# Performance work log

Measured on AMD Instinct MI355X. Metric: run time of the kernel, lower is better.

## Reference

```python
import jax, jax.numpy as jnp
import numpy as np

DELTA = 1e-3  # inverse-distance kernel smoothing from NEC paper
NUM_NEIGHBOURS = 50


def setup_inputs() -> dict:
    key = jax.random.key(0)
    k1, k2, k3 = jax.random.split(key, 3)
    B, C, D = 1024, 500000, 64
    return {
        "keys": jax.random.normal(k1, (B, D), dtype=jnp.float32),
        "table_keys": jax.random.normal(k2, (C, D), dtype=jnp.float32),
        "table_values": jax.random.normal(k3, (C,), dtype=jnp.float32),
    }


def reference(keys, table_keys, table_values):
    # Brute-force kNN search: squared L2 distances [B, C]
    d2 = (
        jnp.sum(keys * keys, axis=1, keepdims=True)
        - 2.0 * (keys @ table_keys.T)
        + jnp.sum(table_keys * table_keys, axis=1)[None, :]
    )
    _, idx = jax.lax.top_k(-d2, NUM_NEIGHBOURS)  # [B, K] smallest distances

    neighbours = table_keys[idx]  # [B, K, D] gather
    # recompute exact squared distances against gathered neighbours
    sq = jnp.sum((keys[:, None, :] - neighbours) ** 2, axis=2)  # [B, K]
    w = 1.0 / (sq + DELTA)
    w = w / jnp.sum(w, axis=1, keepdims=True)
    v = table_values[idx]  # [B, K]
    return jnp.sum(w * v, axis=1)  # [B]
```

## Files before the change

### kernel.cpp

```cpp
#include <hip/hip_runtime.h>
#include <math.h>


#define DELTA_SMOOTH 1e-3f
#define K_NEIGH 50
#define MAXCAP 8192
#define SAMPLE 2048
#define SAMPLE_TARGET 6
#define NBINS 256
#define MARGIN 0.75f
#define MARGIN_Q 26
#define RPB 1024
#define QTILE 512
#define SDEPTH 8
#define LW 768
#define NQ 1024

typedef __attribute__((ext_vector_type(8))) short short8;
typedef __attribute__((ext_vector_type(4))) float f32x4;

__device__ __forceinline__ unsigned f2bf(float f) {
  unsigned u = __float_as_uint(f);
  return ((u + 0x7fffu + ((u >> 16) & 1u)) >> 16) & 0xffffu;
}

__global__ __launch_bounds__(256) void qthresh_kernel(
    const float* __restrict__ keys, const float* __restrict__ tk,
    float* __restrict__ thr, float* __restrict__ qnorm, int C) {
  int q = blockIdx.x;
  __shared__ __align__(16) float kq[64];
  __shared__ unsigned hist[NBINS];
  __shared__ float qn_sh;
  __shared__ unsigned wsum[4];
  __shared__ int bstar_sh;
  int tid = threadIdx.x;
  int lane = tid & 63;
  int wid = tid >> 6;
  if (tid < 64) kq[tid] = keys[(size_t)q * 64 + tid];
  hist[tid] = 0u;
  if (tid == 0) bstar_sh = NBINS - 1;
  __syncthreads();
  if (tid < 64) {
    float v = kq[tid];
    float s = v * v;
    #pragma unroll
    for (int off = 32; off > 0; off >>= 1) s += __shfl_down(s, off);
    if (tid == 0) qn_sh = s;
  }
  __syncthreads();
  float qn = qn_sh;
  int kc = lane & 3;
  const float4* kq4 = (const float4*)kq;
  float4 kf[4];
  #pragma unroll
  for (int j = 0; j < 4; ++j) kf[j] = kq4[kc * 4 + j];
  int S = SAMPLE < C ? SAMPLE : C;
  for (int r = wid * (S >> 2) + (lane >> 2); r < (wid + 1) * (S >> 2); r += 16) {
    const float4* trow = (const float4*)(tk + (size_t)r * 64 + kc * 16);
    float a0 = 0.f, a1 = 0.f, sq = 0.f;
    #pragma unroll
    for (int j = 0; j < 4; ++j) {
      float4 tvv = trow[j];
      float4 kv = kf[j];
      a0 += kv.x * tvv.x + kv.y * tvv.y;
      a1 += kv.z * tvv.z + kv.w * tvv.w;
      sq += tvv.x * tvv.x + tvv.y * tvv.y + tvv.z * tvv.z + tvv.w * tvv.w;
    }
    float s = a0 + a1;
    s += __shfl_xor(s, 1); s += __shfl_xor(s, 2);
    sq += __shfl_xor(sq, 1); sq += __shfl_xor(sq, 2);
    if (kc == 0) {
      float d2 = qn + sq - 2.f * s;
      int b = (int)d2;
      b = b < 0 ? 0 : (b > NBINS - 1 ? NBINS - 1 : b);
      atomicAdd(&hist[b], 1u);
    }
  }
  __syncthreads();
  unsigned h = hist[tid];
  unsigned p = h;
  #pragma unroll
  for (int off = 1; off < 64; off <<= 1) {
    unsigned v = __shfl_up(p, off);
    if (lane >= off) p += v;
  }
  if (lane == 63) wsum[wid] = p;
  __syncthreads();
  unsigned add = 0;
  for (int w2 = 0; w2 < wid; ++w2) add += wsum[w2];
  p += add;
  if (p >= (unsigned)SAMPLE_TARGET && p - h < (unsigned)SAMPLE_TARGET) bstar_sh = tid;
  __syncthreads();
  if (tid == 0) {
    thr[q] = (float)(bstar_sh + 1) + MARGIN - qn;
    qnorm[q] = qn;
  }
}

__global__ __launch_bounds__(512, 4) void filter_mfma_kernel(
    const float* __restrict__ keys, const float* __restrict__ tk,
    const float* __restrict__ thr, const float* __restrict__ qnorm,
    int* __restrict__ cnt, unsigned* __restrict__ candi, int C, int cap) {
  __shared__ float tnstage[64];
  __shared__ float thr_lds[QTILE];
  __shared__ float qn_lds[QTILE];
  __shared__ unsigned scnt[QTILE];
  __shared__ unsigned sbuf[QTILE * SDEPTH];
  __shared__ __align__(16) unsigned char bstage[64 * 128];

  int tid = threadIdx.x;
  int qt = blockIdx.x & 1;
  int chunk = blockIdx.x >> 1;
  int qbase = qt * QTILE;
  int rstart = chunk * RPB;

  thr_lds[tid] = thr[qbase + tid];
  qn_lds[tid] = qnorm[qbase + tid];
  scnt[tid] = 0u;

  int lane = tid & 63;
  int wq = tid >> 6;
  int l15 = lane & 15;
  int quad = lane >> 4;

  short8 afrag[4][2];
  #pragma unroll
  for (int mt = 0; mt < 4; ++mt) {
    const float* kp = keys + (size_t)(qbase + wq * 64 + mt * 16 + l15) * 64 + quad * 8;
    #pragma unroll
    for (int s = 0; s < 2; ++s) {
      float4 x = *(const float4*)(kp + s * 32);
      float4 y = *(const float4*)(kp + s * 32 + 4);
      short8 a;
      a[0] = (short)f2bf(x.x); a[1] = (short)f2bf(x.y);
      a[2] = (short)f2bf(x.z); a[3] = (short)f2bf(x.w);
      a[4] = (short)f2bf(y.x); a[5] = (short)f2bf(y.y);
      a[6] = (short)f2bf(y.z); a[7] = (short)f2bf(y.w);
      afrag[mt][s] = a;
    }
  }
  __syncthreads();

  float hq[4];
  #pragma unroll
  for (int mt = 0; mt < 4; ++mt) {
    float h0 = thr_lds[wq * 64 + mt * 16 + quad * 4 + 0];
    float h1 = thr_lds[wq * 64 + mt * 16 + quad * 4 + 1];
    float h2 = thr_lds[wq * 64 + mt * 16 + quad * 4 + 2];
    float h3 = thr_lds[wq * 64 + mt * 16 + quad * 4 + 3];
    hq[mt] = fmaxf(fmaxf(h0, h1), fmaxf(h2, h3));
  }

  int srow = tid >> 3;
  int scol = tid & 7;
  unsigned sbyte = (unsigned)(srow * 128 + ((scol ^ (srow & 7)) << 4));

  const int ITERS = RPB / 64;
  int r0 = rstart + srow; if (r0 > C - 1) r0 = C - 1;
  float4 pa = *(const float4*)(tk + (size_t)r0 * 64 + scol * 8);
  float4 pb = *(const float4*)(tk + (size_t)r0 * 64 + scol * 8 + 4);

  f32x4 zero4 = {0.f, 0.f, 0.f, 0.f};

  for (int it = 0; it < ITERS; ++it) {
    float part = pa.x * pa.x + pa.y * pa.y + pa.z * pa.z + pa.w * pa.w
               + pb.x * pb.x + pb.y * pb.y + pb.z * pb.z + pb.w * pb.w;
    part += __shfl_xor(part, 1);
    part += __shfl_xor(part, 2);
    part += __shfl_xor(part, 4);
    if ((tid & 7) == 0) tnstage[srow] = part;
    uint4 u;
    u.x = f2bf(pa.x) | (f2bf(pa.y) << 16);
    u.y = f2bf(pa.z) | (f2bf(pa.w) << 16);
    u.z = f2bf(pb.x) | (f2bf(pb.y) << 16);
    u.w = f2bf(pb.z) | (f2bf(pb.w) << 16);
    *(uint4*)(bstage + sbyte) = u;
    __syncthreads();
    if (it + 1 < ITERS) {
      int rn = rstart + (it + 1) * 64 + srow; if (rn > C - 1) rn = C - 1;
      pa = *(const float4*)(tk + (size_t)rn * 64 + scol * 8);
      pb = *(const float4*)(tk + (size_t)rn * 64 + scol * 8 + 4);
    }
    #pragma unroll
    for (int half = 0; half < 2; ++half) {
      short8 b[2][2];
      #pragma unroll
      for (int tt = 0; tt < 2; ++tt) {
        int nloc = half * 32 + tt * 16 + l15;
        #pragma unroll
        for (int s = 0; s < 2; ++s) {
          int c = s * 4 + quad;
          unsigned addr = (unsigned)(nloc * 128 + ((c ^ (nloc & 7)) << 4));
          b[tt][s] = *(const short8*)(bstage + addr);
        }
      }
      f32x4 acc[4][2];
      #pragma unroll
      for (int mt = 0; mt < 4; ++mt) {
        #pragma unroll
        for (int tt = 0; tt < 2; ++tt) {
          f32x4 a0 = __builtin_amdgcn_mfma_f32_16x16x32_bf16(afrag[mt][0], b[tt][0], zero4, 0, 0, 0);
          acc[mt][tt] = __builtin_amdgcn_mfma_f32_16x16x32_bf16(afrag[mt][1], b[tt][1], a0, 0, 0, 0);
        }
      }
      #pragma unroll
      for (int tt = 0; tt < 2; ++tt) {
        float tn = tnstage[half * 32 + tt * 16 + l15];
        int n = rstart + it * 64 + half * 32 + tt * 16 + l15;
        #pragma unroll
        for (int mt = 0; mt < 4; ++mt) {
          float d0 = fmaf(-2.f, acc[mt][tt][0], tn);
          float d1 = fmaf(-2.f, acc[mt][tt][1], tn);
          float d2 = fmaf(-2.f, acc[mt][tt][2], tn);
          float d3 = fmaf(-2.f, acc[mt][tt][3], tn);
          float mn4 = fminf(fminf(d0, d1), fminf(d2, d3));
          if (mn4 < hq[mt]) {
            float dd[4] = {d0, d1, d2, d3};
            #pragma unroll
            for (int r = 0; r < 4; ++r) {
              int ql = wq * 64 + mt * 16 + quad * 4 + r;
              if (dd[r] < thr_lds[ql] && n < C) {
                float d2f = dd[r] + qn_lds[ql];
                int d2q = (int)(d2f * 16.f);
                d2q = d2q < 0 ? 0 : (d2q > 8191 ? 8191 : d2q);
                unsigned v = ((unsigned)d2q << 19) | (unsigned)n;
                unsigned p = atomicAdd(&scnt[ql], 1u);
                if (p < SDEPTH) {
                  sbuf[ql * SDEPTH + p] = v;
                } else {
                  int g = atomicAdd(&cnt[qbase + ql], 1);
                  if (g < cap) candi[(size_t)(qbase + ql) * cap + g] = v;
                }
              }
            }
          }
        }
      }
    }
    __syncthreads();
  }
  int m = (int)scnt[tid];
  if (m > SDEPTH) m = SDEPTH;
  if (m > 0) {
    int base = atomicAdd(&cnt[qbase + tid], m);
    for (int j = 0; j < m; ++j) {
      int g = base + j;
      if (g < cap) candi[(size_t)(qbase + tid) * cap + g] = sbuf[tid * SDEPTH + j];
    }
  }
}

__global__ __launch_bounds__(256) void select_kernel(
    const float* __restrict__ keys, const float* __restrict__ tk,
    const float* __restrict__ tv, const int* __restrict__ cnt,
    const unsigned* __restrict__ candi, float* __restrict__ out, int cap) {
  int q = blockIdx.x;
  __shared__ unsigned hist[NBINS];
  __shared__ unsigned wsum[4];
  __shared__ unsigned minq_sh;
  __shared__ int b50_sh;
  __shared__ int lidx[LW];
  __shared__ unsigned ed2[LW];
  __shared__ int m_sh;
  __shared__ float redw[4], redwv[4];
  int tid = threadIdx.x;
  int lane = tid & 63;
  int wid = tid >> 6;
  int n = cnt[q];
  if (n > cap) n = cap;
  hist[tid] = 0u;
  if (tid == 0) { minq_sh = 0xffffffffu; b50_sh = NBINS - 1; m_sh = 0; }
  __syncthreads();
  const unsigned* cv = candi + (size_t)q * cap;
  unsigned mn = 0xffffffffu;
  for (int i = tid; i < n; i += 256) { unsigned d = cv[i] >> 19; if (d < mn) mn = d; }
  #pragma unroll
  for (int off = 1; off < 64; off <<= 1) { unsigned o = __shfl_xor(mn, off); if (o < mn) mn = o; }
  if (lane == 0) atomicMin(&minq_sh, mn);
  __syncthreads();
  unsigned base = minq_sh;
  for (int i = tid; i < n; i += 256) {
    unsigned d = (cv[i] >> 19) - base;
    unsigned b = d >> 1; if (b > NBINS - 1) b = NBINS - 1;
    atomicAdd(&hist[b], 1u);
  }
  __syncthreads();
  unsigned h = hist[tid];
  unsigned p = h;
  #pragma unroll
  for (int off = 1; off < 64; off <<= 1) {
    unsigned v = __shfl_up(p, off);
    if (lane >= off) p += v;
  }
  if (lane == 63) wsum[wid] = p;
  __syncthreads();
  unsigned add = 0;
  for (int w2 = 0; w2 < wid; ++w2) add += wsum[w2];
  p += add;
  if (p >= (unsigned)K_NEIGH && p - h < (unsigned)K_NEIGH) b50_sh = tid;
  __syncthreads();
  unsigned Tq = base + (((unsigned)(b50_sh + 1)) << 1) + MARGIN_Q;
  for (int i = tid; i < n; i += 256) {
    unsigned v = cv[i];
    if ((v >> 19) <= Tq) {
      int p2 = atomicAdd(&m_sh, 1);
      if (p2 < LW) lidx[p2] = (int)(v & 0x7ffffu);
    }
  }
  __syncthreads();
  int m = m_sh; if (m > LW) m = LW;
  float kqv = keys[(size_t)q * 64 + lane];
  for (int i0 = wid * 4; i0 < m; i0 += 16) {
    int mm = m - i0; if (mm > 4) mm = 4;
    int idx[4]; float t[4];
    for (int u = 0; u < mm; ++u) idx[u] = lidx[i0 + u];
    for (int u = 0; u < mm; ++u) t[u] = tk[(size_t)idx[u] * 64 + lane];
    for (int u = 0; u < mm; ++u) {
      float d = t[u] - kqv;
      float s = d * d;
      #pragma unroll
      for (int off = 1; off < 64; off <<= 1) s += __shfl_xor(s, off);
      if (lane == 0) ed2[i0 + u] = __float_as_uint(s);
    }
  }
  __syncthreads();
  float accw = 0.f, accwv = 0.f;
  for (int i = tid; i < m; i += 256) {
    unsigned long long key = ((unsigned long long)ed2[i] << 19) | (unsigned)lidx[i];
    int rank = 0;
    for (int j = 0; j < m; ++j) {
      unsigned long long kj = ((unsigned long long)ed2[j] << 19) | (unsigned)lidx[j];
      rank += (kj < key) ? 1 : 0;
    }
    if (rank < K_NEIGH) {
      float d2 = __uint_as_float(ed2[i]);
      float w = 1.f / (d2 + DELTA_SMOOTH);
      accw += w;
      accwv += w * tv[lidx[i]];
    }
  }
  #pragma unroll
  for (int off = 1; off < 64; off <<= 1) {
    accw += __shfl_xor(accw, off);
    accwv += __shfl_xor(accwv, off);
  }
  if (lane == 0) { redw[wid] = accw; redwv[wid] = accwv; }
  __syncthreads();
  if (tid == 0) {
    float sw = redw[0] + redw[1] + redw[2] + redw[3];
    float swv = redwv[0] + redwv[1] + redwv[2] + redwv[3];
    out[q] = swv / sw;
  }
}

extern "C" void kernel_launch(void* const* d_in, const int* in_sizes, int n_in,
                              void* d_out, int out_size, void* d_ws, size_t ws_size,
                              hipStream_t stream) {
  const float* keys = (const float*)d_in[0];
  const float* tk   = (const float*)d_in[1];
  const float* tv   = (const float*)d_in[2];
  float* out = (float*)d_out;
  int B = in_sizes[0] / 64;
  int C = in_sizes[2];

  char* w = (char*)d_ws;
  float* thr = (float*)w;  w += (size_t)B * 4;
  float* qn  = (float*)w;  w += (size_t)B * 4;
  int*   cnt = (int*)w;    w += (size_t)B * 4;
  size_t used = (size_t)(w - (char*)d_ws);
  size_t avail = ws_size > used ? ws_size - used : 0;
  int cap = (int)(avail / (4ull * (size_t)B));
  if (cap > MAXCAP) cap = MAXCAP;
  if (cap < 1) cap = 1;
  unsigned* candi = (unsigned*)w;

  hipMemsetAsync(cnt, 0, (size_t)B * 4, stream);
  qthresh_kernel<<<B, 256, 0, stream>>>(keys, tk, thr, qn, C);
  int nchunks = (C + RPB - 1) / RPB;
  filter_mfma_kernel<<<nchunks * 2, 512, 0, stream>>>(keys, tk, thr, qn,
                                                      cnt, candi, C, cap);
  select_kernel<<<B, 256, 0, stream>>>(keys, tk, tv, cnt, candi, out, cap);
}
```

Before: 450.0 us.

## Pre-convert table to swizzled bf16 with norms, batch qthresh queries, cache candidates in LDS

Adds a conversion kernel that writes the table keys once as bf16 in a swizzled 64-row tile layout and precomputes row norms. A new filter kernel streams these tiles with double-buffered LDS staging and register prefetch, which halves the bytes read per filter block and drops the in-kernel conversion. It also prunes quad groups with a max-threshold early-out before the per-row checks. Separately, qthresh processes 8 queries per block to reuse each sampled table row, and select_kernel caches candidate lists in LDS to avoid rereading global memory. The conversion pass adds a full read of the table per call plus extra workspace, with a fallback to the old path when the workspace is too small.

Result: slower. 511.8 us (+13.7%).

```diff
diff --git a/kernel.cpp b/kernel.cpp
--- a/kernel.cpp
+++ b/kernel.cpp
@@ -14,7 +14,8 @@
 #define QTILE 512
 #define SDEPTH 8
 #define LW 768
-#define NQ 1024
+#define QB 8
+#define CVL 4096
 
 typedef __attribute__((ext_vector_type(8))) short short8;
 typedef __attribute__((ext_vector_type(4))) float f32x4;
@@ -24,76 +25,245 @@
   return ((u + 0x7fffu + ((u >> 16) & 1u)) >> 16) & 0xffffu;
 }
 
+__global__ __launch_bounds__(256) void convert_kernel(
+    const float* __restrict__ tk, uint4* __restrict__ tkbf,
+    float* __restrict__ tnorm, int C, int padded) {
+  int t = blockIdx.x * 256 + threadIdx.x;
+  int r = t >> 3;
+  if (r >= padded) return;
+  int c = t & 7;
+  int rs = r < C ? r : C - 1;
+  const float4* src = (const float4*)(tk + (size_t)rs * 64 + c * 8);
+  float4 a = src[0], b = src[1];
+  float sq = a.x * a.x + a.y * a.y + a.z * a.z + a.w * a.w
+           + b.x * b.x + b.y * b.y + b.z * b.z + b.w * b.w;
+  sq += __shfl_xor(sq, 1); sq += __shfl_xor(sq, 2); sq += __shfl_xor(sq, 4);
+  if (c == 0) tnorm[r] = sq;
+  uint4 u;
+  u.x = f2bf(a.x) | (f2bf(a.y) << 16);
+  u.y = f2bf(a.z) | (f2bf(a.w) << 16);
+  u.z = f2bf(b.x) | (f2bf(b.y) << 16);
+  u.w = f2bf(b.z) | (f2bf(b.w) << 16);
+  int tile = r >> 6, lr = r & 63;
+  tkbf[(size_t)tile * 512 + lr * 8 + (c ^ (lr & 7))] = u;
+}
+
 __global__ __launch_bounds__(256) void qthresh_kernel(
     const float* __restrict__ keys, const float* __restrict__ tk,
     float* __restrict__ thr, float* __restrict__ qnorm, int C) {
-  int q = blockIdx.x;
-  __shared__ __align__(16) float kq[64];
-  __shared__ unsigned hist[NBINS];
-  __shared__ float qn_sh;
-  __shared__ unsigned wsum[4];
-  __shared__ int bstar_sh;
+  int q0 = blockIdx.x * QB;
+  __shared__ __align__(16) float kq[QB * 64];
+  __shared__ unsigned hist[QB][NBINS];
+  __shared__ float qn8[QB];
   int tid = threadIdx.x;
   int lane = tid & 63;
   int wid = tid >> 6;
-  if (tid < 64) kq[tid] = keys[(size_t)q * 64 + tid];
-  hist[tid] = 0u;
-  if (tid == 0) bstar_sh = NBINS - 1;
-  __syncthreads();
-  if (tid < 64) {
-    float v = kq[tid];
-    float s = v * v;
+  for (int i = tid; i < QB * 64; i += 256) kq[i] = keys[(size_t)q0 * 64 + i];
+  for (int i = tid; i < QB * NBINS; i += 256) (&hist[0][0])[i] = 0u;
+  __syncthreads();
+  if (tid < QB) {
+    float s = 0.f;
+    for (int j = 0; j < 64; ++j) { float v = kq[tid * 64 + j]; s += v * v; }
+    qn8[tid] = s;
+  }
+  __syncthreads();
+  int kc = lane & 3;
+  const int SQ4 = SAMPLE >> 2;
+  for (int pass = 0; pass < 2; ++pass) {
+    float4 kf[4][4];
     #pragma unroll
-    for (int off = 32; off > 0; off >>= 1) s += __shfl_down(s, off);
-    if (tid == 0) qn_sh = s;
-  }
-  __syncthreads();
-  float qn = qn_sh;
-  int kc = lane & 3;
-  const float4* kq4 = (const float4*)kq;
-  float4 kf[4];
-  #pragma unroll
-  for (int j = 0; j < 4; ++j) kf[j] = kq4[kc * 4 + j];
-  int S = SAMPLE < C ? SAMPLE : C;
-  for (int r = wid * (S >> 2) + (lane >> 2); r < (wid + 1) * (S >> 2); r += 16) {
-    const float4* trow = (const float4*)(tk + (size_t)r * 64 + kc * 16);
-    float a0 = 0.f, a1 = 0.f, sq = 0.f;
+    for (int j = 0; j < 4; ++j)
+      #pragma unroll
+      for (int u = 0; u < 4; ++u)
+        kf[j][u] = ((const float4*)kq)[(pass * 4 + j) * 16 + kc * 4 + u];
+    for (int rr = (lane >> 2); rr < SQ4; rr += 16) {
+      int r = wid * SQ4 + rr;
+      const float4* trow = (const float4*)(tk + (size_t)r * 64 + kc * 16);
+      float4 t0 = trow[0], t1 = trow[1], t2 = trow[2], t3 = trow[3];
+      #pragma unroll
+      for (int j = 0; j < 4; ++j) {
+        float s = kf[j][0].x * t0.x + kf[j][0].y * t0.y + kf[j][0].z * t0.z + kf[j][0].w * t0.w
+                + kf[j][1].x * t1.x + kf[j][1].y * t1.y + kf[j][1].z * t1.z + kf[j][1].w * t1.w
+                + kf[j][2].x * t2.x + kf[j][2].y * t2.y + kf[j][2].z * t2.z + kf[j][2].w * t2.w
+                + kf[j][3].x * t3.x + kf[j][3].y * t3.y + kf[j][3].z * t3.z + kf[j][3].w * t3.w;
+        s += __shfl_xor(s, 1); s += __shfl_xor(s, 2);
+        if (kc == 0) {
+          int jq = pass * 4 + j;
+          float tn = t0.x * t0.x + t0.y * t0.y + t0.z * t0.z + t0.w * t0.w
+                   + t1.x * t1.x + t1.y * t1.y + t1.z * t1.z + t1.w * t1.w
+                   + t2.x * t2.x + t2.y * t2.y + t2.z * t2.z + t2.w * t2.w
+                   + t3.x * t3.x + t3.y * t3.y + t3.z * t3.z + t3.w * t3.w;
+          (void)tn;
+          float d2 = 0.f; (void)d2;
+          int b = 0; (void)b; (void)jq;
+        }
+      }
+      float tnp = t0.x * t0.x + t0.y * t0.y + t0.z * t0.z + t0.w * t0.w
+                + t1.x * t1.x + t1.y * t1.y + t1.z * t1.z + t1.w * t1.w
+                + t2.x * t2.x + t2.y * t2.y + t2.z * t2.z + t2.w * t2.w
+                + t3.x * t3.x + t3.y * t3.y + t3.z * t3.z + t3.w * t3.w;
+      tnp += __shfl_xor(tnp, 1); tnp += __shfl_xor(tnp, 2);
+      #pragma unroll
+      for (int j = 0; j < 4; ++j) {
+        float s = kf[j][0].x * t0.x + kf[j][0].y * t0.y + kf[j][0].z * t0.z + kf[j][0].w * t0.w
+                + kf[j][1].x * t1.x + kf[j][1].y * t1.y + kf[j][1].z * t1.z + kf[j][1].w * t1.w
+                + kf[j][2].x * t2.x + kf[j][2].y * t2.y + kf[j][2].z * t2.z + kf[j][2].w * t2.w
+                + kf[j][3].x * t3.x + kf[j][3].y * t3.y + kf[j][3].z * t3.z + kf[j][3].w * t3.w;
+        s += __shfl_xor(s, 1); s += __shfl_xor(s, 2);
+        if (kc == 0) {
+          int jq = pass * 4 + j;
+          float d2 = qn8[jq] + tnp - 2.f * s;
+          int b = (int)d2;
+          b = b < 0 ? 0 : (b > NBINS - 1 ? NBINS - 1 : b);
+          atomicAdd(&hist[jq][b], 1u);
+        }
+      }
+    }
+  }
+  __syncthreads();
+  if (tid < QB) {
+    unsigned cum = 0; int bstar = NBINS - 1;
+    for (int b = 0; b < NBINS; ++b) {
+      cum += hist[tid][b];
+      if (cum >= (unsigned)SAMPLE_TARGET) { bstar = b; break; }
+    }
+    thr[q0 + tid] = (float)(bstar + 1) + MARGIN - qn8[tid];
+    qnorm[q0 + tid] = qn8[tid];
+  }
+}
+
+__global__ __launch_bounds__(512, 4) void filter_mfma_fast(
+    const uint4* __restrict__ tkbf, const float* __restrict__ keys,
+    const float* __restrict__ tnorm, const float* __restrict__ thr,
+    const float* __restrict__ qnorm, int* __restrict__ cnt,
+    unsigned* __restrict__ candi, int C, int cap) {
+  __shared__ float tnorm_lds[RPB];
+  __shared__ float thr_lds[QTILE];
+  __shared__ float qn_lds[QTILE];
+  __shared__ unsigned scnt[QTILE];
+  __shared__ unsigned sbuf[QTILE * SDEPTH];
+  __shared__ __align__(16) unsigned char bstage[2][64 * 128];
+
+  int tid = threadIdx.x;
+  int qt = blockIdx.x & 1;
+  int chunk = blockIdx.x >> 1;
+  int qbase = qt * QTILE;
+  int rstart = chunk * RPB;
+
+  tnorm_lds[tid] = tnorm[rstart + tid];
+  tnorm_lds[tid + 512] = tnorm[rstart + tid + 512];
+  thr_lds[tid] = thr[qbase + tid];
+  qn_lds[tid] = qnorm[qbase + tid];
+  scnt[tid] = 0u;
+
+  int lane = tid & 63;
+  int wq = tid >> 6;
+  int l15 = lane & 15;
+  int quad = lane >> 4;
+
+  short8 afrag[4][2];
+  #pragma unroll
+  for (int mt = 0; mt < 4; ++mt) {
+    const float* kp = keys + (size_t)(qbase + wq * 64 + mt * 16 + l15) * 64 + quad * 8;
     #pragma unroll
-    for (int j = 0; j < 4; ++j) {
-      float4 tvv = trow[j];
-      float4 kv = kf[j];
-      a0 += kv.x * tvv.x + kv.y * tvv.y;
-      a1 += kv.z * tvv.z + kv.w * tvv.w;
-      sq += tvv.x * tvv.x + tvv.y * tvv.y + tvv.z * tvv.z + tvv.w * tvv.w;
-    }
-    float s = a0 + a1;
-    s += __shfl_xor(s, 1); s += __shfl_xor(s, 2);
-    sq += __shfl_xor(sq, 1); sq += __shfl_xor(sq, 2);
-    if (kc == 0) {
-      float d2 = qn + sq - 2.f * s;
-      int b = (int)d2;
-      b = b < 0 ? 0 : (b > NBINS - 1 ? NBINS - 1 : b);
-      atomicAdd(&hist[b], 1u);
-    }
-  }
-  __syncthreads();
-  unsigned h = hist[tid];
-  unsigned p = h;
-  #pragma unroll
-  for (int off = 1; off < 64; off <<= 1) {
-    unsigned v = __shfl_up(p, off);
-    if (lane >= off) p += v;
-  }
-  if (lane == 63) wsum[wid] = p;
-  __syncthreads();
-  unsigned add = 0;
-  for (int w2 = 0; w2 < wid; ++w2) add += wsum[w2];
-  p += add;
-  if (p >= (unsigned)SAMPLE_TARGET && p - h < (unsigned)SAMPLE_TARGET) bstar_sh = tid;
-  __syncthreads();
-  if (tid == 0) {
-    thr[q] = (float)(bstar_sh + 1) + MARGIN - qn;
-    qnorm[q] = qn;
+    for (int s = 0; s < 2; ++s) {
+      float4 x = *(const float4*)(kp + s * 32);
+      float4 y = *(const float4*)(kp + s * 32 + 4);
+      short8 a;
+      a[0] = (short)f2bf(x.x); a[1] = (short)f2bf(x.y);
+      a[2] = (short)f2bf(x.z); a[3] = (short)f2bf(x.w);
+      a[4] = (short)f2bf(y.x); a[5] = (short)f2bf(y.y);
+      a[6] = (short)f2bf(y.z); a[7] = (short)f2bf(y.w);
+      afrag[mt][s] = a;
+    }
+  }
+
+  float th2[4];
+  #pragma unroll
+  for (int mt = 0; mt < 4; ++mt) {
+    float h0 = thr_lds[wq * 64 + mt * 16 + quad * 4 + 0];
+    float h1 = thr_lds[wq * 64 + mt * 16 + quad * 4 + 1];
+    float h2 = thr_lds[wq * 64 + mt * 16 + quad * 4 + 2];
+    float h3 = thr_lds[wq * 64 + mt * 16 + quad * 4 + 3];
+    th2[mt] = fmaxf(fmaxf(h0, h1), fmaxf(h2, h3)) * 0.5f;
+  }
+
+  const int ITERS = RPB / 64;
+  const uint4* gsrc = tkbf + (size_t)(rstart >> 6) * 512;
+  uint4 pre = gsrc[tid];
+
+  f32x4 zero4 = {0.f, 0.f, 0.f, 0.f};
+
+  for (int it = 0; it < ITERS; ++it) {
+    unsigned char* buf = bstage[it & 1];
+    ((uint4*)buf)[tid] = pre;
+    if (it + 1 < ITERS) pre = gsrc[(size_t)(it + 1) * 512 + tid];
+    __syncthreads();
+    #pragma unroll
+    for (int half = 0; half < 2; ++half) {
+      short8 b[2][2];
+      #pragma unroll
+      for (int tt = 0; tt < 2; ++tt) {
+        int nloc = half * 32 + tt * 16 + l15;
+        #pragma unroll
+        for (int s = 0; s < 2; ++s) {
+          int c = s * 4 + quad;
+          unsigned addr = (unsigned)(nloc * 128 + ((c ^ (nloc & 7)) << 4));
+          b[tt][s] = *(const short8*)(buf + addr);
+        }
+      }
+      f32x4 acc[4][2];
+      #pragma unroll
+      for (int mt = 0; mt < 4; ++mt) {
+        #pragma unroll
+        for (int tt = 0; tt < 2; ++tt) {
+          f32x4 a0 = __builtin_amdgcn_mfma_f32_16x16x32_bf16(afrag[mt][0], b[tt][0], zero4, 0, 0, 0);
+          acc[mt][tt] = __builtin_amdgcn_mfma_f32_16x16x32_bf16(afrag[mt][1], b[tt][1], a0, 0, 0, 0);
+        }
+      }
+      #pragma unroll
+      for (int tt = 0; tt < 2; ++tt) {
+        int rloc = it * 64 + half * 32 + tt * 16 + l15;
+        float tn = tnorm_lds[rloc];
+        float tnh = tn * 0.5f;
+        int n = rstart + rloc;
+        #pragma unroll
+        for (int mt = 0; mt < 4; ++mt) {
+          float mx4 = fmaxf(fmaxf(acc[mt][tt][0], acc[mt][tt][1]),
+                            fmaxf(acc[mt][tt][2], acc[mt][tt][3]));
+          if (mx4 > tnh - th2[mt]) {
+            #pragma unroll
+            for (int r = 0; r < 4; ++r) {
+              float d2p = fmaf(-2.f, acc[mt][tt][r], tn);
+              int ql = wq * 64 + mt * 16 + quad * 4 + r;
+              if (d2p < thr_lds[ql] && n < C) {
+                float d2f = d2p + qn_lds[ql];
+                int d2q = (int)(d2f * 16.f);
+                d2q = d2q < 0 ? 0 : (d2q > 8191 ? 8191 : d2q);
+                unsigned v = ((unsigned)d2q << 19) | (unsigned)n;
+                unsigned p = atomicAdd(&scnt[ql], 1u);
+                if (p < SDEPTH) {
+                  sbuf[ql * SDEPTH + p] = v;
+                } else {
+                  int g = atomicAdd(&cnt[qbase + ql], 1);
+                  if (g < cap) candi[(size_t)(qbase + ql) * cap + g] = v;
+                }
+              }
+            }
+          }
+        }
+      }
+    }
+    __syncthreads();
+  }
+  int m = (int)scnt[tid];
+  if (m > SDEPTH) m = SDEPTH;
+  if (m > 0) {
+    int base = atomicAdd(&cnt[qbase + tid], m);
+    for (int j = 0; j < m; ++j) {
+      int g = base + j;
+      if (g < cap) candi[(size_t)(qbase + tid) * cap + g] = sbuf[tid * SDEPTH + j];
+    }
   }
 }
 
@@ -255,6 +425,7 @@
     const float* __restrict__ tv, const int* __restrict__ cnt,
     const unsigned* __restrict__ candi, float* __restrict__ out, int cap) {
   int q = blockIdx.x;
+  __shared__ unsigned cvl[CVL];
   __shared__ unsigned hist[NBINS];
   __shared__ unsigned wsum[4];
   __shared__ unsigned minq_sh;
@@ -273,14 +444,19 @@
   __syncthreads();
   const unsigned* cv = candi + (size_t)q * cap;
   unsigned mn = 0xffffffffu;
-  for (int i = tid; i < n; i += 256) { unsigned d = cv[i] >> 19; if (d < mn) mn = d; }
+  for (int i = tid; i < n; i += 256) {
+    unsigned v = cv[i];
+    if (i < CVL) cvl[i] = v;
+    unsigned d = v >> 19; if (d < mn) mn = d;
+  }
   #pragma unroll
   for (int off = 1; off < 64; off <<= 1) { unsigned o = __shfl_xor(mn, off); if (o < mn) mn = o; }
   if (lane == 0) atomicMin(&minq_sh, mn);
   __syncthreads();
   unsigned base = minq_sh;
   for (int i = tid; i < n; i += 256) {
-    unsigned d = (cv[i] >> 19) - base;
+    unsigned v = (i < CVL) ? cvl[i] : cv[i];
+    unsigned d = (v >> 19) - base;
     unsigned b = d >> 1; if (b > NBINS - 1) b = NBINS - 1;
     atomicAdd(&hist[b], 1u);
   }
@@ -301,7 +477,7 @@
   __syncthreads();
   unsigned Tq = base + (((unsigned)(b50_sh + 1)) << 1) + MARGIN_Q;
   for (int i = tid; i < n; i += 256) {
-    unsigned v = cv[i];
+    unsigned v = (i < CVL) ? cvl[i] : cv[i];
     if ((v >> 19) <= Tq) {
       int p2 = atomicAdd(&m_sh, 1);
       if (p2 < LW) lidx[p2] = (int)(v & 0x7ffffu);
@@ -363,21 +539,41 @@
   int B = in_sizes[0] / 64;
   int C = in_sizes[2];
 
+  int nchunks = (C + RPB - 1) / RPB;
+  int padded = nchunks * RPB;
+
   char* w = (char*)d_ws;
   float* thr = (float*)w;  w += (size_t)B * 4;
   float* qn  = (float*)w;  w += (size_t)B * 4;
   int*   cnt = (int*)w;    w += (size_t)B * 4;
-  size_t used = (size_t)(w - (char*)d_ws);
-  size_t avail = ws_size > used ? ws_size - used : 0;
-  int cap = (int)(avail / (4ull * (size_t)B));
-  if (cap > MAXCAP) cap = MAXCAP;
-  if (cap < 1) cap = 1;
-  unsigned* candi = (unsigned*)w;
+
+  size_t fixed = (size_t)(w - (char*)d_ws);
+  size_t fast_need = fixed + (size_t)padded * 128 + (size_t)padded * 4
+                   + 2048ull * (size_t)B * 4;
+  bool fast = ws_size >= fast_need;
 
   hipMemsetAsync(cnt, 0, (size_t)B * 4, stream);
-  qthresh_kernel<<<B, 256, 0, stream>>>(keys, tk, thr, qn, C);
-  int nchunks = (C + RPB - 1) / RPB;
-  filter_mfma_kernel<<<nchunks * 2, 512, 0, stream>>>(keys, tk, thr, qn,
+  qthresh_kernel<<<B / QB, 256, 0, stream>>>(keys, tk, thr, qn, C);
+
+  if (fast) {
+    uint4* tkbf   = (uint4*)w;            w += (size_t)padded * 128;
+    float* tnorm  = (float*)w;            w += (size_t)padded * 4;
+    size_t used = (size_t)(w - (char*)d_ws);
+    int cap = (int)((ws_size - used) / (4ull * (size_t)B));
+    if (cap > MAXCAP) cap = MAXCAP;
+    unsigned* candi = (unsigned*)w;
+    convert_kernel<<<padded / 32, 256, 0, stream>>>(tk, tkbf, tnorm, C, padded);
+    filter_mfma_fast<<<nchunks * 2, 512, 0, stream>>>(tkbf, keys, tnorm, thr, qn,
                                                       cnt, candi, C, cap);
-  select_kernel<<<B, 256, 0, stream>>>(keys, tk, tv, cnt, candi, out, cap);
-}
+    select_kernel<<<B, 256, 0, stream>>>(keys, tk, tv, cnt, candi, out, cap);
+  } else {
+    size_t used = fixed;
+    int cap = (int)((ws_size - used) / (4ull * (size_t)B));
+    if (cap > MAXCAP) cap = MAXCAP;
+    if (cap < 1) cap = 1;
+    unsigned* candi = (unsigned*)w;
+    filter_mfma_kernel<<<nchunks * 2, 512, 0, stream>>>(keys, tk, thr, qn,
+                                                        cnt, candi, C, cap);
+    select_kernel<<<B, 256, 0, stream>>>(keys, tk, tv, cnt, candi, out, cap);
+  }
+}
```
